# Kernel tuning notes

Measured on AMD Instinct MI355X. Metric: run time of the kernel, lower is better.

The kernel has to match this reference:

```python
import jax, jax.numpy as jnp
import numpy as np

DIM = 64          # d_model
D_INNER = 128     # 2 * DIM (mamba expand=2)
D_STATE = 16
D_CONV = 4
DT_RANK = 4       # ceil(DIM / 16)


def setup_inputs() -> dict:
    key = jax.random.key(0)
    ks = jax.random.split(key, 8)
    s = 0.05
    f32 = jnp.float32
    return {
        "x": jax.random.normal(ks[0], (2, DIM, 96, 96), f32),
        # GroupNorm(1, dim)
        "gn_gamma": jnp.ones((DIM,), f32),
        "gn_beta": jnp.zeros((DIM,), f32),
        # Mamba params
        "W_in": (jax.random.normal(ks[1], (2 * D_INNER, DIM), f32) * s),
        "b_in": jnp.zeros((2 * D_INNER,), f32),
        "conv_w": (jax.random.normal(ks[2], (D_INNER, 1, D_CONV), f32) * s),
        "conv_b": jnp.zeros((D_INNER,), f32),
        "W_xproj": (jax.random.normal(ks[3], (DT_RANK + 2 * D_STATE, D_INNER), f32) * s),
        "W_dt": (jax.random.normal(ks[4], (D_INNER, DT_RANK), f32) * s),
        "b_dt": jnp.full((D_INNER,), -4.6, f32),  # softplus(-4.6) ~ 0.01
        "A_log": jnp.log(jnp.broadcast_to(jnp.arange(1, D_STATE + 1, dtype=f32), (D_INNER, D_STATE))),
        "Dp": jnp.ones((D_INNER,), f32),
        "W_out": (jax.random.normal(ks[5], (DIM, D_INNER), f32) * s),
        "b_out": jnp.zeros((DIM,), f32),
        # proj: Conv2d(dim, dim, 1) + BatchNorm2d(dim) eval-mode + GELU
        "proj_w": (jax.random.normal(ks[6], (DIM, DIM), f32) * s),
        "proj_b": jnp.zeros((DIM,), f32),
        "bn_gamma": jnp.ones((DIM,), f32),
        "bn_beta": jnp.zeros((DIM,), f32),
        "bn_mean": jnp.zeros((DIM,), f32),
        "bn_var": jnp.ones((DIM,), f32),
    }


def _mamba(u, W_in, b_in, conv_w, conv_b, W_xproj, W_dt, b_dt, A_log, Dp, W_out, b_out):
    # u: [B, L, DIM]
    xz = u @ W_in.T + b_in                      # [B, L, 2*D_INNER]
    x, z = jnp.split(xz, 2, axis=-1)            # each [B, L, D_INNER]
    # depthwise causal conv over L
    xc = jnp.transpose(x, (0, 2, 1))            # [B, D_INNER, L]
    xc = jax.lax.conv_general_dilated(
        xc, conv_w, (1,), [(D_CONV - 1, 0)],
        dimension_numbers=("NCH", "OIH", "NCH"), feature_group_count=D_INNER)
    x = jax.nn.silu(jnp.transpose(xc, (0, 2, 1)) + conv_b)   # [B, L, D_INNER]
    # input-dependent dt, B, C
    dbc = x @ W_xproj.T                          # [B, L, DT_RANK + 2*D_STATE]
    dt = dbc[..., :DT_RANK]
    Bm = dbc[..., DT_RANK:DT_RANK + D_STATE]     # [B, L, D_STATE]
    Cm = dbc[..., DT_RANK + D_STATE:]            # [B, L, D_STATE]
    dt = jax.nn.softplus(dt @ W_dt.T + b_dt)     # [B, L, D_INNER]
    A = -jnp.exp(A_log)                          # [D_INNER, D_STATE]
    deltaA = jnp.exp(dt[..., None] * A)                          # [B, L, D_INNER, D_STATE]
    deltaBu = dt[..., None] * Bm[:, :, None, :] * x[..., None]   # [B, L, D_INNER, D_STATE]
    # parallel linear recurrence h_t = a_t * h_{t-1} + b_t, h_0 = 0
    def comb(e1, e2):
        a1, b1 = e1
        a2, b2 = e2
        return a1 * a2, a2 * b1 + b2
    _, h = jax.lax.associative_scan(comb, (deltaA, deltaBu), axis=1)
    y = jnp.einsum("blds,bls->bld", h, Cm) + x * Dp
    y = y * jax.nn.silu(z)
    return y @ W_out.T + b_out                   # [B, L, DIM]


def reference(x, gn_gamma, gn_beta, W_in, b_in, conv_w, conv_b, W_xproj, W_dt, b_dt,
              A_log, Dp, W_out, b_out, proj_w, proj_b, bn_gamma, bn_beta, bn_mean, bn_var):
    B, C, H, W = x.shape
    # GroupNorm(1, C): normalize over (C, H, W) per sample, biased var
    mu = x.mean(axis=(1, 2, 3), keepdims=True)
    var = x.var(axis=(1, 2, 3), keepdims=True)
    xn = (x - mu) / jnp.sqrt(var + 1e-5)
    xn = xn * gn_gamma[None, :, None, None] + gn_beta[None, :, None, None]
    xn = jnp.clip(xn, -10.0, 10.0)
    res = xn
    seq = jnp.transpose(xn, (0, 2, 3, 1)).reshape(B, H * W, C)
    y = _mamba(seq, W_in, b_in, conv_w, conv_b, W_xproj, W_dt, b_dt, A_log, Dp, W_out, b_out)
    y2d = jnp.transpose(y.reshape(B, H, W, C), (0, 3, 1, 2))
    # proj: 1x1 conv + eval BatchNorm + exact GELU
    p = jnp.einsum("oc,bchw->bohw", proj_w, y2d) + proj_b[None, :, None, None]
    p = (p - bn_mean[None, :, None, None]) / jnp.sqrt(bn_var[None, :, None, None] + 1e-5)
    p = p * bn_gamma[None, :, None, None] + bn_beta[None, :, None, None]
    p = jax.nn.gelu(p, approximate=False)
    return jnp.clip(res + p, -10.0, 10.0)
```

## Files before the change

### kernel.cpp

```cpp
#include <hip/hip_runtime.h>
#include <math.h>

#define DIMC 64
#define DIN  128
#define LSEQ 9216
#define NPB  (DIMC*LSEQ)
#define NCH  192
#define CTL  48
#define NCHAIN 4096
#define LOG2E 1.44269504088896340736f

__device__ __forceinline__ float siluf(float v)    { return v / (1.f + __expf(-v)); }
__device__ __forceinline__ float softplusf(float v){ return (v > 15.f) ? v : __logf(1.f + __expf(v)); }
__device__ __forceinline__ float clip10(float v)   { return fminf(10.f, fmaxf(-10.f, v)); }
__device__ __forceinline__ float getc(const float4 v, int k) {
  return (k == 0) ? v.x : (k == 1) ? v.y : (k == 2) ? v.z : v.w;
}

__global__ void k_init(const float* __restrict__ x, float* __restrict__ sums,
                       const float* __restrict__ W_in, const float* __restrict__ proj_w,
                       const float* __restrict__ W_out, const float* __restrict__ b_out,
                       const float* __restrict__ proj_b, const float* __restrict__ W_xproj,
                       const float* __restrict__ W_dt,
                       float* __restrict__ Wtp, float* __restrict__ Mtp, float* __restrict__ bp,
                       float* __restrict__ Wbtd2, float* __restrict__ Wbc) {
  int bx = blockIdx.x, by = blockIdx.y;
  int t = threadIdx.x;
  if (bx < 256) {
    const float* xb = x + (size_t)by * NPB;
    float s = 0.f, s2 = 0.f;
    for (int i = bx * 256 + t; i < NPB; i += 65536) {
      float v = xb[i]; s += v; s2 = fmaf(v, v, s2);
    }
    __shared__ float l1[256], l2[256];
    l1[t] = s; l2[t] = s2; __syncthreads();
    for (int off = 128; off > 0; off >>= 1) {
      if (t < off) { l1[t] += l1[t + off]; l2[t] += l2[t + off]; }
      __syncthreads();
    }
    if (t == 0) { atomicAdd(&sums[2*by], l1[0]); atomicAdd(&sums[2*by+1], l2[0]); }
    return;
  }
  if (by != 0) return;
  int i = (bx - 256) * 256 + t;
  if (i < 16384) {
    int k = i >> 8, cc = i & 255, c = cc & 127, h = cc >> 7;
    Wtp[(k * 128 + c) * 2 + h] = W_in[(c + 128 * h) * 64 + k];
    return;
  }
  int j = i - 16384;
  if (j < 8192) {
    int d = j >> 6, o = j & 63, o32 = o & 31, h = o >> 5;
    float a = 0.f;
    for (int c = 0; c < 64; c++) a = fmaf(proj_w[o * 64 + c], W_out[c * DIN + d], a);
    Mtp[(d * 32 + o32) * 2 + h] = a;
    return;
  }
  int k2 = j - 8192;
  if (k2 < 64) {
    float a = proj_b[k2];
    for (int c = 0; c < 64; c++) a = fmaf(proj_w[k2 * 64 + c], b_out[c], a);
    bp[k2] = a;
    return;
  }
  int m = j - 8256;
  if (m < 16384) {
    int k = m >> 7, cc = m & 127, c = cc & 63, h = cc >> 6;
    float v = 0.f;
    #pragma unroll
    for (int r = 0; r < 4; r++) v = fmaf(W_dt[(c + 64 * h) * 4 + r], W_xproj[r * DIN + k], v);
    Wbtd2[(k * 64 + c) * 2 + h] = v;
    return;
  }
  int m2 = m - 16384;
  if (m2 < 4096) {
    int k = m2 >> 5, jj = m2 & 31;
    Wbc[m2] = W_xproj[(4 + jj) * DIN + k];
  }
}

__global__ void k_norm(const float* __restrict__ x, const float* __restrict__ gam,
                       const float* __restrict__ bet, const float* __restrict__ sums,
                       float* __restrict__ seq, float* __restrict__ res) {
  int b = blockIdx.y, l0 = blockIdx.x * 64;
  float mean = sums[2*b] * (1.f / NPB);
  float var  = sums[2*b+1] * (1.f / NPB) - mean * mean;
  float inv  = rsqrtf(var + 1e-5f);
  __shared__ float tile[64][65];
  int t = threadIdx.x;
  int lr = t & 63, cg = t >> 6;
  #pragma unroll
  for (int i = 0; i < 16; i++) {
    int c = i * 4 + cg;
    size_t idx = ((size_t)(b * DIMC + c)) * LSEQ + l0 + lr;
    float v = x[idx];
    v = (v - mean) * inv * gam[c] + bet[c];
    v = clip10(v);
    res[idx] = v;
    tile[c][lr] = v;
  }
  __syncthreads();
  int cc = t & 63, lg = t >> 6;
  #pragma unroll
  for (int i = 0; i < 16; i++) {
    int l = i * 4 + lg;
    seq[((size_t)(b * LSEQ + l0 + l)) * DIMC + cc] = tile[cc][l];
  }
}

__global__ void __launch_bounds__(256) k_mid(
    const float* __restrict__ seq, const float* __restrict__ Wtp,
    const float* __restrict__ b_in, const float* __restrict__ conv_w,
    const float* __restrict__ conv_b, const float* __restrict__ Wbtd2,
    const float* __restrict__ Wbc, const float* __restrict__ b_dt,
    float* __restrict__ xs, float* __restrict__ zo, float* __restrict__ dt,
    float* __restrict__ Bm, float* __restrict__ Cm) {
  int row0 = blockIdx.x * 16;
  int t = threadIdx.x;
  __shared__ float sq[19 * 64];
  __shared__ float xt[16 * DIN];

  for (int i = t; i < 19 * 16; i += 256) {
    int r = i >> 4, k4 = i & 15;
    int rr = row0 - 3 + r; if (rr < 0) rr = 0;
    *(float4*)(sq + r * 64 + k4 * 4) = *(const float4*)(seq + (size_t)rr * DIMC + k4 * 4);
  }
  __syncthreads();

  {
    int c = t & 127;
    int rh = t >> 7;
    float bx_ = b_in[c], bz_ = b_in[c + 128];
    float ax[11], az[11];
    #pragma unroll
    for (int j = 0; j < 11; j++) { ax[j] = bx_; az[j] = bz_; }
    const float4* sq4 = (const float4*)sq;
    const float2* W2  = (const float2*)Wtp;
    for (int k4 = 0; k4 < 16; k4++) {
      float2 w0 = W2[(size_t)(k4 * 4 + 0) * 128 + c];
      float2 w1 = W2[(size_t)(k4 * 4 + 1) * 128 + c];
      float2 w2 = W2[(size_t)(k4 * 4 + 2) * 128 + c];
      float2 w3 = W2[(size_t)(k4 * 4 + 3) * 128 + c];
      #pragma unroll
      for (int j = 0; j < 11; j++) {
        float4 sv = sq4[(rh * 8 + j) * 16 + k4];
        ax[j] = fmaf(w0.x, sv.x, ax[j]); az[j] = fmaf(w0.y, sv.x, az[j]);
        ax[j] = fmaf(w1.x, sv.y, ax[j]); az[j] = fmaf(w1.y, sv.y, az[j]);
        ax[j] = fmaf(w2.x, sv.z, ax[j]); az[j] = fmaf(w2.y, sv.z, az[j]);
        ax[j] = fmaf(w3.x, sv.w, ax[j]); az[j] = fmaf(w3.y, sv.w, az[j]);
      }
    }
    if ((row0 % LSEQ) == 0 && rh == 0) { ax[0] = 0.f; ax[1] = 0.f; ax[2] = 0.f; }
    float4 cw = *(const float4*)(conv_w + c * 4);
    float cb = conv_b[c];
    #pragma unroll
    for (int i2 = 0; i2 < 8; i2++) {
      float v = cb;
      v = fmaf(ax[i2 + 0], cw.x, v);
      v = fmaf(ax[i2 + 1], cw.y, v);
      v = fmaf(ax[i2 + 2], cw.z, v);
      v = fmaf(ax[i2 + 3], cw.w, v);
      float sv_ = siluf(v);
      int r = rh * 8 + i2;
      xs[(size_t)(row0 + r) * DIN + c] = sv_;
      xt[r * DIN + c] = sv_;
      zo[(size_t)(row0 + r) * DIN + c] = az[i2 + 3];
    }
  }
  __syncthreads();

  const float4* xt4 = (const float4*)xt;

  {
    int cd = t & 63, rg = t >> 6;
    float acc0[4], acc1[4];
    float bd0 = b_dt[cd], bd1 = b_dt[cd + 64];
    #pragma unroll
    for (int r = 0; r < 4; r++) { acc0[r] = bd0; acc1[r] = bd1; }
    const float2* Wd2 = (const float2*)Wbtd2;
    for (int k4 = 0; k4 < 32; k4++) {
      float4 v0 = xt4[(rg * 4 + 0) * 32 + k4];
      float4 v1 = xt4[(rg * 4 + 1) * 32 + k4];
      float4 v2 = xt4[(rg * 4 + 2) * 32 + k4];
      float4 v3 = xt4[(rg * 4 + 3) * 32 + k4];
      #pragma unroll
      for (int kk = 0; kk < 4; kk++) {
        float2 w = Wd2[(size_t)(k4 * 4 + kk) * 64 + cd];
        float s0 = getc(v0, kk), s1 = getc(v1, kk), s2 = getc(v2, kk), s3 = getc(v3, kk);
        acc0[0] = fmaf(w.x, s0, acc0[0]); acc1[0] = fmaf(w.y, s0, acc1[0]);
        acc0[1] = fmaf(w.x, s1, acc0[1]); acc1[1] = fmaf(w.y, s1, acc1[1]);
        acc0[2] = fmaf(w.x, s2, acc0[2]); acc1[2] = fmaf(w.y, s2, acc1[2]);
        acc0[3] = fmaf(w.x, s3, acc0[3]); acc1[3] = fmaf(w.y, s3, acc1[3]);
      }
    }
    #pragma unroll
    for (int r = 0; r < 4; r++) {
      size_t ro = (size_t)(row0 + rg * 4 + r) * DIN;
      dt[ro + cd]      = softplusf(acc0[r]);
      dt[ro + cd + 64] = softplusf(acc1[r]);
    }
  }

  {
    int cb2 = t & 31, rg = t >> 5;
    float a0 = 0.f, a1 = 0.f;
    for (int k4 = 0; k4 < 32; k4++) {
      float4 v0 = xt4[(rg * 2 + 0) * 32 + k4];
      float4 v1 = xt4[(rg * 2 + 1) * 32 + k4];
      #pragma unroll
      for (int kk = 0; kk < 4; kk++) {
        float w = Wbc[(k4 * 4 + kk) * 32 + cb2];
        a0 = fmaf(w, getc(v0, kk), a0);
        a1 = fmaf(w, getc(v1, kk), a1);
      }
    }
    size_t r0 = (size_t)row0 + rg * 2;
    float* dst = (cb2 < 16) ? (Bm + r0 * 16 + cb2) : (Cm + r0 * 16 + (cb2 - 16));
    dst[0]  = a0;
    dst[16] = a1;
  }
}

__global__ void __launch_bounds__(512) k_scanA(
    const float* __restrict__ dt, const float* __restrict__ Bmat,
    const float* __restrict__ xs, const float* __restrict__ A_log,
    float* __restrict__ Ap, float* __restrict__ Bg) {
  int chunk = blockIdx.x, b = blockIdx.y;
  int t = threadIdx.x;
  int d = t >> 2, q = t & 3;
  const float* al = A_log + d * 16 + q * 4;
  float a0 = -__expf(al[0]) * LOG2E, a1 = -__expf(al[1]) * LOG2E;
  float a2 = -__expf(al[2]) * LOG2E, a3 = -__expf(al[3]) * LOG2E;
  size_t base = (size_t)b * LSEQ + (size_t)chunk * CTL;
  const float* dtp = dt + base * DIN + d;
  const float* xsp = xs + base * DIN + d;
  const float4* bp4 = (const float4*)(Bmat + base * 16 + q * 4);
  float h0 = 0.f, h1 = 0.f, h2 = 0.f, h3 = 0.f;
  float p0 = 1.f, p1 = 1.f, p2 = 1.f, p3 = 1.f;
  #pragma unroll 4
  for (int i = 0; i < CTL; i++) {
    float dtv = dtp[(size_t)i * DIN];
    float xv  = xsp[(size_t)i * DIN];
    float4 bA = bp4[i * 4];
    float u = dtv * xv;
    float e;
    e = exp2f(dtv * a0); h0 = fmaf(e, h0, u * bA.x); p0 *= e;
    e = exp2f(dtv * a1); h1 = fmaf(e, h1, u * bA.y); p1 *= e;
    e = exp2f(dtv * a2); h2 = fmaf(e, h2, u * bA.z); p2 *= e;
    e = exp2f(dtv * a3); h3 = fmaf(e, h3, u * bA.w); p3 *= e;
  }
  size_t idx = (size_t)chunk * NCHAIN + (size_t)(b * DIN + d) * 16 + q * 4;
  *(float4*)(Ap + idx) = make_float4(p0, p1, p2, p3);
  *(float4*)(Bg + idx) = make_float4(h0, h1, h2, h3);
}

__global__ void k_scanB(const float* __restrict__ Ap, const float* __restrict__ Bg,
                        float* __restrict__ hinit) {
  int chain = blockIdx.x * 64 + threadIdx.x;
  float h = 0.f;
  for (int c = 0; c < NCH; c++) {
    size_t idx = (size_t)c * NCHAIN + chain;
    hinit[idx] = h;
    h = fmaf(Ap[idx], h, Bg[idx]);
  }
}

__global__ void __launch_bounds__(512) k_scanC(
    const float* __restrict__ dt, const float* __restrict__ Bmat,
    const float* __restrict__ Cmat, const float* __restrict__ xs,
    const float* __restrict__ z, const float* __restrict__ A_log,
    const float* __restrict__ Dp, const float* __restrict__ hinit,
    const float* __restrict__ Mtp, const float* __restrict__ bp,
    const float* __restrict__ bn_g, const float* __restrict__ bn_bt,
    const float* __restrict__ bn_m, const float* __restrict__ bn_v,
    const float* __restrict__ res, float* __restrict__ out) {
  int chunk = blockIdx.x, b = blockIdx.y;
  int t = threadIdx.x;
  __shared__ float ytile[CTL * DIN];
  __shared__ float trans[64 * 52];
  {
    int d = t >> 2, q = t & 3;
    const float* al = A_log + d * 16 + q * 4;
    float a0 = -__expf(al[0]) * LOG2E, a1 = -__expf(al[1]) * LOG2E;
    float a2 = -__expf(al[2]) * LOG2E, a3 = -__expf(al[3]) * LOG2E;
    float dp = Dp[d];
    size_t base = (size_t)b * LSEQ + (size_t)chunk * CTL;
    const float* dtp = dt + base * DIN + d;
    const float* xsp = xs + base * DIN + d;
    const float* zp  = z  + base * DIN + d;
    const float4* bp4 = (const float4*)(Bmat + base * 16 + q * 4);
    const float4* cp4 = (const float4*)(Cmat + base * 16 + q * 4);
    size_t idx = (size_t)chunk * NCHAIN + (size_t)(b * DIN + d) * 16 + q * 4;
    float4 hv = *(const float4*)(hinit + idx);
    float h0 = hv.x, h1 = hv.y, h2 = hv.z, h3 = hv.w;
    #pragma unroll 2
    for (int i = 0; i < CTL; i++) {
      float dtv = dtp[(size_t)i * DIN];
      float xv  = xsp[(size_t)i * DIN];
      float4 bA = bp4[i * 4];
      float4 cA = cp4[i * 4];
      float u = dtv * xv;
      float e, p;
      e = exp2f(dtv * a0); h0 = fmaf(e, h0, u * bA.x); p = h0 * cA.x;
      e = exp2f(dtv * a1); h1 = fmaf(e, h1, u * bA.y); p = fmaf(h1, cA.y, p);
      e = exp2f(dtv * a2); h2 = fmaf(e, h2, u * bA.z); p = fmaf(h2, cA.z, p);
      e = exp2f(dtv * a3); h3 = fmaf(e, h3, u * bA.w); p = fmaf(h3, cA.w, p);
      p += __shfl_xor(p, 1);
      p += __shfl_xor(p, 2);
      if (q == 0) {
        float zv = zp[(size_t)i * DIN];
        ytile[i * DIN + d] = (p + xv * dp) * siluf(zv);
      }
    }
  }
  __syncthreads();

  {
    int op = t & 31, rg = t >> 5;
    float acc0[3], acc1[3];
    float b0 = bp[op], b1 = bp[op + 32];
    #pragma unroll
    for (int r = 0; r < 3; r++) { acc0[r] = b0; acc1[r] = b1; }
    const float4* yt4 = (const float4*)ytile;
    const float2* M2  = (const float2*)Mtp;
    for (int k4 = 0; k4 < 32; k4++) {
      float4 v0 = yt4[(rg * 3 + 0) * 32 + k4];
      float4 v1 = yt4[(rg * 3 + 1) * 32 + k4];
      float4 v2 = yt4[(rg * 3 + 2) * 32 + k4];
      #pragma unroll
      for (int kk = 0; kk < 4; kk++) {
        float2 w = M2[(size_t)(k4 * 4 + kk) * 32 + op];
        float s0 = getc(v0, kk), s1 = getc(v1, kk), s2 = getc(v2, kk);
        acc0[0] = fmaf(w.x, s0, acc0[0]); acc1[0] = fmaf(w.y, s0, acc1[0]);
        acc0[1] = fmaf(w.x, s1, acc0[1]); acc1[1] = fmaf(w.y, s1, acc1[1]);
        acc0[2] = fmaf(w.x, s2, acc0[2]); acc1[2] = fmaf(w.y, s2, acc1[2]);
      }
    }
    float g0 = bn_g[op], bt0 = bn_bt[op], mu0 = bn_m[op];
    float iv0 = rsqrtf(bn_v[op] + 1e-5f);
    float g1 = bn_g[op + 32], bt1 = bn_bt[op + 32], mu1 = bn_m[op + 32];
    float iv1 = rsqrtf(bn_v[op + 32] + 1e-5f);
    __syncthreads();
    #pragma unroll
    for (int r = 0; r < 3; r++) {
      int row = rg * 3 + r;
      float a = (acc0[r] - mu0) * iv0 * g0 + bt0;
      a = 0.5f * a * (1.f + erff(a * 0.70710678118654752f));
      trans[op * 52 + row] = a;
      float a2 = (acc1[r] - mu1) * iv1 * g1 + bt1;
      a2 = 0.5f * a2 * (1.f + erff(a2 * 0.70710678118654752f));
      trans[(op + 32) * 52 + row] = a2;
    }
  }
  __syncthreads();

  int l0c = chunk * CTL;
  for (int task = t; task < 768; task += 512) {
    int c = task / 12, f = task - c * 12;
    float4 vv = *(const float4*)(trans + c * 52 + f * 4);
    size_t gi = ((size_t)(b * DIMC + c)) * LSEQ + l0c + f * 4;
    const float4 rv = *(const float4*)(res + gi);
    float4 o;
    o.x = clip10(rv.x + vv.x);
    o.y = clip10(rv.y + vv.y);
    o.z = clip10(rv.z + vv.z);
    o.w = clip10(rv.w + vv.w);
    *(float4*)(out + gi) = o;
  }
}

extern "C" void kernel_launch(void* const* d_in, const int* in_sizes, int n_in,
                              void* d_out, int out_size, void* d_ws, size_t ws_size,
                              hipStream_t stream) {
  const float* x       = (const float*)d_in[0];
  const float* gn_g    = (const float*)d_in[1];
  const float* gn_b    = (const float*)d_in[2];
  const float* W_in    = (const float*)d_in[3];
  const float* b_in    = (const float*)d_in[4];
  const float* conv_w  = (const float*)d_in[5];
  const float* conv_b  = (const float*)d_in[6];
  const float* W_xproj = (const float*)d_in[7];
  const float* W_dt    = (const float*)d_in[8];
  const float* b_dt    = (const float*)d_in[9];
  const float* A_log   = (const float*)d_in[10];
  const float* Dp      = (const float*)d_in[11];
  const float* W_out   = (const float*)d_in[12];
  const float* b_out   = (const float*)d_in[13];
  const float* proj_w  = (const float*)d_in[14];
  const float* proj_b  = (const float*)d_in[15];
  const float* bn_g    = (const float*)d_in[16];
  const float* bn_bt   = (const float*)d_in[17];
  const float* bn_m    = (const float*)d_in[18];
  const float* bn_v    = (const float*)d_in[19];

  float* ws = (float*)d_ws;
  float* sums = ws;
  float* seq  = ws + 64;
  float* res  = seq + 1179648;
  float* zbuf = res + 1179648;
  float* xsb  = zbuf + 2359296;
  float* dtb  = xsb + 2359296;
  float* Bmb  = dtb + 2359296;
  float* Cmb  = Bmb + 294912;
  float* Wtp  = Cmb + 294912;
  float* Mtp  = Wtp + 16384;
  float* bp   = Mtp + 8192;
  float* Wbtd2= bp + 64;
  float* Wbc  = Wbtd2 + 16384;
  float* Bgb  = Wbc + 4096;
  float* hib  = Bgb + 786432;
  float* Apb  = seq;

  hipMemsetAsync(sums, 0, 64 * sizeof(float), stream);

  k_init<<<dim3(433, 2), 256, 0, stream>>>(x, sums, W_in, proj_w, W_out, b_out, proj_b,
                                           W_xproj, W_dt, Wtp, Mtp, bp, Wbtd2, Wbc);
  k_norm<<<dim3(144, 2), 256, 0, stream>>>(x, gn_g, gn_b, sums, seq, res);
  k_mid<<<1152, 256, 0, stream>>>(seq, Wtp, b_in, conv_w, conv_b, Wbtd2, Wbc, b_dt,
                                  xsb, zbuf, dtb, Bmb, Cmb);
  k_scanA<<<dim3(NCH, 2), 512, 0, stream>>>(dtb, Bmb, xsb, A_log, Apb, Bgb);
  k_scanB<<<64, 64, 0, stream>>>(Apb, Bgb, hib);
  k_scanC<<<dim3(NCH, 2), 512, 0, stream>>>(dtb, Bmb, Cmb, xsb, zbuf, A_log, Dp, hib,
                                            Mtp, bp, bn_g, bn_bt, bn_m, bn_v, res,
                                            (float*)d_out);
}
```

Measured before the change: 248.8 us.

## Give each thread one in_proj output column across all rows, remap scan thread layout

In the mid kernel's in-projection, each thread now owns a single output column (x or z half) over all 19 rows, instead of computing paired x/z columns over 11 rows. This removes the overlapping halo rows the old two-row-group split computed twice, and the weight layout becomes plain transposed. It also splits the conv/SiLU and z stores by thread half. The cost is a larger accumulator array per thread and divergent work between the two halves. Separately, the scanA thread mapping changes so consecutive threads cover consecutive channels, which affects how dt/xs loads coalesce.

Result: slower. 255.1 us (+2.5%).

```diff
diff --git a/kernel.cpp b/kernel.cpp
--- a/kernel.cpp
+++ b/kernel.cpp
@@ -22,7 +22,7 @@
                        const float* __restrict__ W_out, const float* __restrict__ b_out,
                        const float* __restrict__ proj_b, const float* __restrict__ W_xproj,
                        const float* __restrict__ W_dt,
-                       float* __restrict__ Wtp, float* __restrict__ Mtp, float* __restrict__ bp,
+                       float* __restrict__ Wt, float* __restrict__ Mtp, float* __restrict__ bp,
                        float* __restrict__ Wbtd2, float* __restrict__ Wbc) {
   int bx = blockIdx.x, by = blockIdx.y;
   int t = threadIdx.x;
@@ -44,8 +44,8 @@
   if (by != 0) return;
   int i = (bx - 256) * 256 + t;
   if (i < 16384) {
-    int k = i >> 8, cc = i & 255, c = cc & 127, h = cc >> 7;
-    Wtp[(k * 128 + c) * 2 + h] = W_in[(c + 128 * h) * 64 + k];
+    int k = i >> 8, c = i & 255;
+    Wt[i] = W_in[c * 64 + k];
     return;
   }
   int j = i - 16384;
@@ -109,13 +109,14 @@
 }
 
 __global__ void __launch_bounds__(256) k_mid(
-    const float* __restrict__ seq, const float* __restrict__ Wtp,
+    const float* __restrict__ seq, const float* __restrict__ Wt,
     const float* __restrict__ b_in, const float* __restrict__ conv_w,
     const float* __restrict__ conv_b, const float* __restrict__ Wbtd2,
     const float* __restrict__ Wbc, const float* __restrict__ b_dt,
     float* __restrict__ xs, float* __restrict__ zo, float* __restrict__ dt,
     float* __restrict__ Bm, float* __restrict__ Cm) {
   int row0 = blockIdx.x * 16;
+  int l0 = row0 % LSEQ;
   int t = threadIdx.x;
   __shared__ float sq[19 * 64];
   __shared__ float xt[16 * DIN];
@@ -128,43 +129,46 @@
   __syncthreads();
 
   {
-    int c = t & 127;
-    int rh = t >> 7;
-    float bx_ = b_in[c], bz_ = b_in[c + 128];
-    float ax[11], az[11];
-    #pragma unroll
-    for (int j = 0; j < 11; j++) { ax[j] = bx_; az[j] = bz_; }
+    int c = t;
+    float bi = b_in[c];
+    float a[19];
+    #pragma unroll
+    for (int r = 0; r < 19; r++) a[r] = bi;
     const float4* sq4 = (const float4*)sq;
-    const float2* W2  = (const float2*)Wtp;
+    #pragma unroll 4
     for (int k4 = 0; k4 < 16; k4++) {
-      float2 w0 = W2[(size_t)(k4 * 4 + 0) * 128 + c];
-      float2 w1 = W2[(size_t)(k4 * 4 + 1) * 128 + c];
-      float2 w2 = W2[(size_t)(k4 * 4 + 2) * 128 + c];
-      float2 w3 = W2[(size_t)(k4 * 4 + 3) * 128 + c];
-      #pragma unroll
-      for (int j = 0; j < 11; j++) {
-        float4 sv = sq4[(rh * 8 + j) * 16 + k4];
-        ax[j] = fmaf(w0.x, sv.x, ax[j]); az[j] = fmaf(w0.y, sv.x, az[j]);
-        ax[j] = fmaf(w1.x, sv.y, ax[j]); az[j] = fmaf(w1.y, sv.y, az[j]);
-        ax[j] = fmaf(w2.x, sv.z, ax[j]); az[j] = fmaf(w2.y, sv.z, az[j]);
-        ax[j] = fmaf(w3.x, sv.w, ax[j]); az[j] = fmaf(w3.y, sv.w, az[j]);
-      }
-    }
-    if ((row0 % LSEQ) == 0 && rh == 0) { ax[0] = 0.f; ax[1] = 0.f; ax[2] = 0.f; }
-    float4 cw = *(const float4*)(conv_w + c * 4);
-    float cb = conv_b[c];
-    #pragma unroll
-    for (int i2 = 0; i2 < 8; i2++) {
-      float v = cb;
-      v = fmaf(ax[i2 + 0], cw.x, v);
-      v = fmaf(ax[i2 + 1], cw.y, v);
-      v = fmaf(ax[i2 + 2], cw.z, v);
-      v = fmaf(ax[i2 + 3], cw.w, v);
-      float sv_ = siluf(v);
-      int r = rh * 8 + i2;
-      xs[(size_t)(row0 + r) * DIN + c] = sv_;
-      xt[r * DIN + c] = sv_;
-      zo[(size_t)(row0 + r) * DIN + c] = az[i2 + 3];
+      float w0 = Wt[(k4 * 4 + 0) * 256 + c];
+      float w1 = Wt[(k4 * 4 + 1) * 256 + c];
+      float w2 = Wt[(k4 * 4 + 2) * 256 + c];
+      float w3 = Wt[(k4 * 4 + 3) * 256 + c];
+      #pragma unroll
+      for (int r = 0; r < 19; r++) {
+        float4 v = sq4[r * 16 + k4];
+        a[r] = fmaf(w0, v.x, a[r]);
+        a[r] = fmaf(w1, v.y, a[r]);
+        a[r] = fmaf(w2, v.z, a[r]);
+        a[r] = fmaf(w3, v.w, a[r]);
+      }
+    }
+    if (c < DIN) {
+      if (l0 == 0) { a[0] = 0.f; a[1] = 0.f; a[2] = 0.f; }
+      float4 cw = *(const float4*)(conv_w + c * 4);
+      float cb = conv_b[c];
+      #pragma unroll
+      for (int i2 = 0; i2 < 16; i2++) {
+        float v = cb;
+        v = fmaf(a[i2 + 0], cw.x, v);
+        v = fmaf(a[i2 + 1], cw.y, v);
+        v = fmaf(a[i2 + 2], cw.z, v);
+        v = fmaf(a[i2 + 3], cw.w, v);
+        float sv_ = siluf(v);
+        xs[(size_t)(row0 + i2) * DIN + c] = sv_;
+        xt[i2 * DIN + c] = sv_;
+      }
+    } else {
+      int cz = c - DIN;
+      #pragma unroll
+      for (int i2 = 0; i2 < 16; i2++) zo[(size_t)(row0 + i2) * DIN + cz] = a[i2 + 3];
     }
   }
   __syncthreads();
@@ -227,7 +231,7 @@
     float* __restrict__ Ap, float* __restrict__ Bg) {
   int chunk = blockIdx.x, b = blockIdx.y;
   int t = threadIdx.x;
-  int d = t >> 2, q = t & 3;
+  int d = t & 127, q = t >> 7;
   const float* al = A_log + d * 16 + q * 4;
   float a0 = -__expf(al[0]) * LOG2E, a1 = -__expf(al[1]) * LOG2E;
   float a2 = -__expf(al[2]) * LOG2E, a3 = -__expf(al[3]) * LOG2E;
@@ -402,8 +406,8 @@
   float* dtb  = xsb + 2359296;
   float* Bmb  = dtb + 2359296;
   float* Cmb  = Bmb + 294912;
-  float* Wtp  = Cmb + 294912;
-  float* Mtp  = Wtp + 16384;
+  float* Wt   = Cmb + 294912;
+  float* Mtp  = Wt + 16384;
   float* bp   = Mtp + 8192;
   float* Wbtd2= bp + 64;
   float* Wbc  = Wbtd2 + 16384;
@@ -414,9 +418,9 @@
   hipMemsetAsync(sums, 0, 64 * sizeof(float), stream);
 
   k_init<<<dim3(433, 2), 256, 0, stream>>>(x, sums, W_in, proj_w, W_out, b_out, proj_b,
-                                           W_xproj, W_dt, Wtp, Mtp, bp, Wbtd2, Wbc);
+                                           W_xproj, W_dt, Wt, Mtp, bp, Wbtd2, Wbc);
   k_norm<<<dim3(144, 2), 256, 0, stream>>>(x, gn_g, gn_b, sums, seq, res);
-  k_mid<<<1152, 256, 0, stream>>>(seq, Wtp, b_in, conv_w, conv_b, Wbtd2, Wbc, b_dt,
+  k_mid<<<1152, 256, 0, stream>>>(seq, Wt, b_in, conv_w, conv_b, Wbtd2, Wbc, b_dt,
                                   xsb, zbuf, dtb, Bmb, Cmb);
   k_scanA<<<dim3(NCH, 2), 512, 0, stream>>>(dtb, Bmb, xsb, A_log, Apb, Bgb);
   k_scanB<<<64, 64, 0, stream>>>(Apb, Bgb, hib);
```
